# Kernel tuning notes

Measured on AMD Instinct MI355X. Metric: run time of the kernel, lower is better.

Reference implementation:

```python
import jax, jax.numpy as jnp
import numpy as np

B, T, C, V = 8, 2048, 1024, 32000


def setup_inputs() -> dict:
    key = jax.random.key(0)
    ks = jax.random.split(key, 12)
    s = 1.0 / np.sqrt(C)
    return {
        "input_tokens": jax.random.randint(ks[0], (B, T), 0, V),
        "xx_init": jnp.zeros((B, C), jnp.float32),
        "aa_init": jnp.zeros((B, C), jnp.float32),
        "bb_init": jnp.zeros((B, C), jnp.float32),
        "pp_init": jnp.zeros((B, C), jnp.float32),  # with aa=bb=0 this is equivalent to -inf init
        "emb": jax.random.normal(ks[1], (V, C), jnp.float32) * 0.02,
        "time_mix_k": jax.random.uniform(ks[2], (C,), jnp.float32),
        "time_mix_v": jax.random.uniform(ks[3], (C,), jnp.float32),
        "time_mix_r": jax.random.uniform(ks[4], (C,), jnp.float32),
        "time_decay": jax.random.normal(ks[5], (C,), jnp.float32) * 0.1,
        "time_first": jax.random.normal(ks[6], (C,), jnp.float32) * 0.1,
        "Wk": jax.random.normal(ks[7], (C, C), jnp.float32) * s,
        "Wv": jax.random.normal(ks[8], (C, C), jnp.float32) * s,
        "Wr": jax.random.normal(ks[9], (C, C), jnp.float32) * s,
        "Wo": jax.random.normal(ks[10], (C, C), jnp.float32) * s,
    }


def _wkv_scan(k, v, aa0, bb0, pp0, w, u):
    """Numerically-stable RWKV WKV recurrence.
    k, v: [T, B, C]; aa0/bb0/pp0: [B, C]; w (decay, negative), u (bonus): [C]."""
    def step(carry, kv):
        aa, bb, pp = carry
        kt, vt = kv
        ww = u + kt
        p = jnp.maximum(pp, ww)
        e1 = jnp.exp(pp - p)
        e2 = jnp.exp(ww - p)
        wkv = (e1 * aa + e2 * vt) / (e1 * bb + e2)
        ww2 = pp + w
        p2 = jnp.maximum(ww2, kt)
        e1b = jnp.exp(ww2 - p2)
        e2b = jnp.exp(kt - p2)
        return (e1b * aa + e2b * vt, e1b * bb + e2b, p2), wkv
    (aa, bb, pp), out = jax.lax.scan(step, (aa0, bb0, pp0), (k, v))
    return out, aa, bb, pp


def _forward(input_tokens, xx_init, aa_init, bb_init, pp_init, emb,
             time_mix_k, time_mix_v, time_mix_r, time_decay, time_first,
             Wk, Wv, Wr, Wo):
    x = emb[input_tokens]                                   # [B, T, C]
    xprev = jnp.concatenate([xx_init[:, None, :], x[:, :-1]], axis=1)  # token shift
    xk = x * time_mix_k + xprev * (1.0 - time_mix_k)
    xv = x * time_mix_v + xprev * (1.0 - time_mix_v)
    xr = x * time_mix_r + xprev * (1.0 - time_mix_r)
    k = jnp.einsum("btc,dc->btd", xk, Wk)
    v = jnp.einsum("btc,dc->btd", xv, Wv)
    r = jax.nn.sigmoid(jnp.einsum("btc,dc->btd", xr, Wr))
    w = -jnp.exp(time_decay)                                # per-channel decay
    u = time_first
    wkv, _, _, _ = _wkv_scan(jnp.swapaxes(k, 0, 1), jnp.swapaxes(v, 0, 1),
                             aa_init, bb_init, pp_init, w, u)
    wkv = jnp.swapaxes(wkv, 0, 1)                           # [B, T, C]
    rwkv = jnp.einsum("btc,dc->btd", r * wkv, Wo)
    e1 = rwkv[:, -1]          # final-step state
    e2 = rwkv.mean(axis=1)    # time-averaged state
    hx = (e1 + e2) * 0.5
    return jnp.stack([hx, hx])  # (hx, cx) stacked -> [2, B, C]


def reference(input_tokens, xx_init, aa_init, bb_init, pp_init, emb,
              time_mix_k, time_mix_v, time_mix_r, time_decay, time_first,
              Wk, Wv, Wr, Wo):
    return _forward(input_tokens, xx_init, aa_init, bb_init, pp_init, emb,
                    time_mix_k, time_mix_v, time_mix_r, time_decay, time_first,
                    Wk, Wv, Wr, Wo)
```

## Files before the change

kernel.cpp:

```cpp
#include <hip/hip_runtime.h>

#define Bdim 8
#define Tdim 2048
#define Cdim 1024
#define CHUNK 64
#define NCHUNK 32
#define BC (Bdim*Cdim)

typedef float floatx4 __attribute__((ext_vector_type(4)));
typedef _Float16 half8 __attribute__((ext_vector_type(8)));
typedef _Float16 half4v __attribute__((ext_vector_type(4)));
typedef _Float16 half2v __attribute__((ext_vector_type(2)));

__device__ __forceinline__ void load16(const void* g, void* l) {
    __builtin_amdgcn_global_load_lds(
        (const __attribute__((address_space(1))) void*)g,
        (__attribute__((address_space(3))) void*)l, 16, 0, 0);
}

__global__ __launch_bounds__(256) void mix_wconv(const int* __restrict__ tokens,
                                                 const float* __restrict__ xx_init,
                                                 const float* __restrict__ emb,
                                                 const float* __restrict__ tmk,
                                                 const float* __restrict__ tmv,
                                                 const float* __restrict__ tmr,
                                                 const float* __restrict__ Wk,
                                                 const float* __restrict__ Wv,
                                                 const float* __restrict__ Wr,
                                                 _Float16* __restrict__ xk,
                                                 _Float16* __restrict__ xv,
                                                 _Float16* __restrict__ xr,
                                                 _Float16* __restrict__ Wh) {
    int blk = blockIdx.x;
    if (blk < Bdim * Tdim) {
        int row = blk;
        int b = row >> 11;
        int t = row & (Tdim - 1);
        const float* cur = emb + (size_t)tokens[row] * Cdim;
        const float* prv = (t == 0) ? (xx_init + (size_t)b * Cdim)
                                    : (emb + (size_t)tokens[row - 1] * Cdim);
        int c = threadIdx.x * 4;
        float4 cu = *reinterpret_cast<const float4*>(cur + c);
        float4 pv = *reinterpret_cast<const float4*>(prv + c);
        float4 mk = *reinterpret_cast<const float4*>(tmk + c);
        float4 mv = *reinterpret_cast<const float4*>(tmv + c);
        float4 mr = *reinterpret_cast<const float4*>(tmr + c);
        float cf[4] = {cu.x, cu.y, cu.z, cu.w};
        float pf[4] = {pv.x, pv.y, pv.z, pv.w};
        float mkf[4] = {mk.x, mk.y, mk.z, mk.w};
        float mvf[4] = {mv.x, mv.y, mv.z, mv.w};
        float mrf[4] = {mr.x, mr.y, mr.z, mr.w};
        half4v hk, hv, hr;
        #pragma unroll
        for (int j = 0; j < 4; j++) {
            hk[j] = (_Float16)(mkf[j] * cf[j] + (1.0f - mkf[j]) * pf[j]);
            hv[j] = (_Float16)(mvf[j] * cf[j] + (1.0f - mvf[j]) * pf[j]);
            hr[j] = (_Float16)(mrf[j] * cf[j] + (1.0f - mrf[j]) * pf[j]);
        }
        size_t o = (size_t)row * Cdim + c;
        *reinterpret_cast<half4v*>(xk + o) = hk;
        *reinterpret_cast<half4v*>(xv + o) = hv;
        *reinterpret_cast<half4v*>(xr + o) = hr;
    } else {
        int idx2 = blk - Bdim * Tdim;
        int which = idx2 >> 10;
        const float* W = which == 0 ? Wk : (which == 1 ? Wv : Wr);
        _Float16* dst = Wh + (size_t)which * Cdim * Cdim;
        int i = ((idx2 & 1023) * 256 + threadIdx.x) * 4;
        float4 f = *reinterpret_cast<const float4*>(W + i);
        half4v h;
        h[0] = (_Float16)f.x; h[1] = (_Float16)f.y; h[2] = (_Float16)f.z; h[3] = (_Float16)f.w;
        *reinterpret_cast<half4v*>(dst + i) = h;
    }
}

__global__ __launch_bounds__(512, 2) void gemm_kvr(const _Float16* __restrict__ xk,
                                                   const _Float16* __restrict__ xv,
                                                   const _Float16* __restrict__ xr,
                                                   const _Float16* __restrict__ Wh,
                                                   _Float16* __restrict__ ko,
                                                   _Float16* __restrict__ vo,
                                                   _Float16* __restrict__ ro) {
    const int which = blockIdx.y;
    const _Float16* X = which == 0 ? xk : (which == 1 ? xv : xr);
    const _Float16* W = Wh + (size_t)which * Cdim * Cdim;
    _Float16* out     = which == 0 ? ko : (which == 1 ? vo : ro);

    const int lin = blockIdx.x;
    const int xcd = lin & 7;
    const int loc = lin >> 3;
    const int mt = xcd * 8 + (loc >> 2);
    const int nt = loc & 3;
    const int m0 = mt * 256;
    const int n0 = nt * 256;

    __shared__ _Float16 As[4 * 8192];
    __shared__ _Float16 Bs[4 * 8192];

    const int tid = threadIdx.x;
    const int lane = tid & 63;
    const int wave = tid >> 6;
    const int wm = (wave >> 2) * 128;
    const int wn = (wave & 3) * 64;
    const int lr = lane & 15;
    const int lk = lane >> 4;
    const int sw = (lr >> 1) & 3;

    const _Float16* Asrc = X + (size_t)m0 * Cdim;
    const _Float16* Bsrc = W + (size_t)n0 * Cdim;

    floatx4 acc[8][4] = {};

    auto stageA = [&](int kt) {
        const int p = kt & 3;
        const int k0 = kt * 32;
        #pragma unroll
        for (int i = 0; i < 2; i++) {
            int e = i * 512 + tid;
            int r = e >> 2;
            int cp = e & 3;
            int cl = cp ^ ((r >> 1) & 3);
            load16(Asrc + (size_t)r * Cdim + k0 + cl * 8, (char*)(As + p * 8192) + e * 16);
        }
    };
    auto stageB = [&](int kt) {
        const int p = kt & 3;
        const int k0 = kt * 32;
        #pragma unroll
        for (int i = 0; i < 2; i++) {
            int e = i * 512 + tid;
            int r = e >> 2;
            int cp = e & 3;
            int cl = cp ^ ((r >> 1) & 3);
            load16(Bsrc + (size_t)r * Cdim + k0 + cl * 8, (char*)(Bs + p * 8192) + e * 16);
        }
    };

    auto ktile = [&](int kt, bool st) {
        const int p = kt & 3;
        const _Float16* ap = As + p * 8192 + (wm + lr) * 32 + (lk ^ sw) * 8;
        const _Float16* bp = Bs + p * 8192 + (wn + lr) * 32 + (lk ^ sw) * 8;
        half8 af[8], bf[4];
        #pragma unroll
        for (int mi = 0; mi < 4; mi++)
            af[mi] = *reinterpret_cast<const half8*>(ap + mi * 512);
        #pragma unroll
        for (int ni = 0; ni < 4; ni++)
            bf[ni] = *reinterpret_cast<const half8*>(bp + ni * 512);
        if (st) stageA(kt + 3);
        __builtin_amdgcn_s_barrier();
        asm volatile("s_waitcnt lgkmcnt(0)" ::: "memory");
        __builtin_amdgcn_sched_barrier(0);
        __builtin_amdgcn_s_setprio(1);
        #pragma unroll
        for (int mi = 0; mi < 4; mi++)
            #pragma unroll
            for (int ni = 0; ni < 4; ni++)
                acc[mi][ni] = __builtin_amdgcn_mfma_f32_16x16x32_f16(af[mi], bf[ni], acc[mi][ni], 0, 0, 0);
        __builtin_amdgcn_s_setprio(0);
        __builtin_amdgcn_sched_barrier(0);
        __builtin_amdgcn_s_barrier();
        #pragma unroll
        for (int mi = 4; mi < 8; mi++)
            af[mi] = *reinterpret_cast<const half8*>(ap + mi * 512);
        if (st) stageB(kt + 3);
        __builtin_amdgcn_s_barrier();
        asm volatile("s_waitcnt lgkmcnt(0)" ::: "memory");
        __builtin_amdgcn_sched_barrier(0);
        __builtin_amdgcn_s_setprio(1);
        #pragma unroll
        for (int mi = 4; mi < 8; mi++)
            #pragma unroll
            for (int ni = 0; ni < 4; ni++)
                acc[mi][ni] = __builtin_amdgcn_mfma_f32_16x16x32_f16(af[mi], bf[ni], acc[mi][ni], 0, 0, 0);
        __builtin_amdgcn_s_setprio(0);
        __builtin_amdgcn_sched_barrier(0);
    };

    stageA(0); stageB(0); stageA(1); stageB(1); stageA(2); stageB(2);
    asm volatile("s_waitcnt vmcnt(8)" ::: "memory");
    __builtin_amdgcn_s_barrier();

    for (int kt = 0; kt < 29; ++kt) {
        ktile(kt, true);
        asm volatile("s_waitcnt vmcnt(8)" ::: "memory");
        __builtin_amdgcn_s_barrier();
    }
    ktile(29, false);
    asm volatile("s_waitcnt vmcnt(4)" ::: "memory");
    __builtin_amdgcn_s_barrier();
    ktile(30, false);
    asm volatile("s_waitcnt vmcnt(0)" ::: "memory");
    __builtin_amdgcn_s_barrier();
    ktile(31, false);

    #pragma unroll
    for (int mi = 0; mi < 8; mi++) {
        #pragma unroll
        for (int ni = 0; ni < 4; ni++) {
            #pragma unroll
            for (int reg = 0; reg < 4; reg++) {
                int mm = m0 + wm + mi * 16 + (lane >> 4) * 4 + reg;
                int nn = n0 + wn + ni * 16 + (lane & 15);
                float v = acc[mi][ni][reg];
                if (which == 2) v = 1.0f / (1.0f + __expf(-v));
                out[(size_t)mm * Cdim + nn] = (_Float16)v;
            }
        }
    }
}

__global__ __launch_bounds__(256) void scan_pass1(const _Float16* __restrict__ kb,
                                                  const _Float16* __restrict__ vb,
                                                  const float* __restrict__ tdecay,
                                                  float* __restrict__ tot_a,
                                                  float* __restrict__ tot_b,
                                                  float* __restrict__ tot_p) {
    const int idx = blockIdx.x * 256 + threadIdx.x;
    const int j  = idx >> 12;
    const int pc = idx & 4095;
    const int bc = pc * 2;
    const int b  = bc >> 10;
    const int c  = bc & (Cdim - 1);
    const float w0 = -__expf(tdecay[c]);
    const float w1 = -__expf(tdecay[c + 1]);
    const size_t base = ((size_t)(b * Tdim + j * CHUNK)) * Cdim + c;
    float aa0 = 0.0f, bb0 = 0.0f, pp0 = -1e30f;
    float aa1 = 0.0f, bb1 = 0.0f, pp1 = -1e30f;
    const _Float16* kp = kb + base;
    const _Float16* vp = vb + base;
    #pragma unroll 4
    for (int t = 0; t < CHUNK; t++) {
        half2v k2 = *reinterpret_cast<const half2v*>(kp + (size_t)t * Cdim);
        half2v v2 = *reinterpret_cast<const half2v*>(vp + (size_t)t * Cdim);
        {
            float kt = (float)k2[0], vt = (float)v2[0];
            float ww2 = pp0 + w0;
            float p2 = fmaxf(ww2, kt);
            float e1 = __expf(ww2 - p2);
            float e2 = __expf(kt - p2);
            aa0 = e1 * aa0 + e2 * vt; bb0 = e1 * bb0 + e2; pp0 = p2;
        }
        {
            float kt = (float)k2[1], vt = (float)v2[1];
            float ww2 = pp1 + w1;
            float p2 = fmaxf(ww2, kt);
            float e1 = __expf(ww2 - p2);
            float e2 = __expf(kt - p2);
            aa1 = e1 * aa1 + e2 * vt; bb1 = e1 * bb1 + e2; pp1 = p2;
        }
    }
    int o = j * BC + bc;
    *reinterpret_cast<float2*>(tot_a + o) = make_float2(aa0, aa1);
    *reinterpret_cast<float2*>(tot_b + o) = make_float2(bb0, bb1);
    *reinterpret_cast<float2*>(tot_p + o) = make_float2(pp0, pp1);
}

__global__ __launch_bounds__(256) void scan_pass2c(const _Float16* __restrict__ kb,
                                                   const _Float16* __restrict__ vb,
                                                   const _Float16* __restrict__ rb,
                                                   const float* __restrict__ tdecay,
                                                   const float* __restrict__ tfirst,
                                                   const float* __restrict__ aa_init,
                                                   const float* __restrict__ bb_init,
                                                   const float* __restrict__ pp_init,
                                                   const float* __restrict__ tot_a,
                                                   const float* __restrict__ tot_b,
                                                   const float* __restrict__ tot_p,
                                                   float* __restrict__ partial,
                                                   float* __restrict__ ylast) {
    const int idx = blockIdx.x * 256 + threadIdx.x;
    const int j  = idx >> 12;
    const int pc = idx & 4095;
    const int bc = pc * 2;
    const int b  = bc >> 10;
    const int c  = bc & (Cdim - 1);
    const float w0 = -__expf(tdecay[c]);
    const float w1 = -__expf(tdecay[c + 1]);
    const float wL0 = w0 * (float)CHUNK;
    const float wL1 = w1 * (float)CHUNK;
    const float u0 = tfirst[c], u1 = tfirst[c + 1];

    float2 A = *reinterpret_cast<const float2*>(aa_init + bc);
    float2 Bv = *reinterpret_cast<const float2*>(bb_init + bc);
    float2 P = *reinterpret_cast<const float2*>(pp_init + bc);
    float aa0 = A.x, bb0 = Bv.x, pp0 = P.x;
    float aa1 = A.y, bb1 = Bv.y, pp1 = P.y;
    for (int jj = 0; jj < j; jj++) {
        int o = jj * BC + bc;
        float2 ta = *reinterpret_cast<const float2*>(tot_a + o);
        float2 tb = *reinterpret_cast<const float2*>(tot_b + o);
        float2 tp = *reinterpret_cast<const float2*>(tot_p + o);
        {
            float px = pp0 + wL0;
            float q = fmaxf(px, tp.x);
            float e1 = __expf(px - q), e2 = __expf(tp.x - q);
            aa0 = e1 * aa0 + e2 * ta.x; bb0 = e1 * bb0 + e2 * tb.x; pp0 = q;
        }
        {
            float px = pp1 + wL1;
            float q = fmaxf(px, tp.y);
            float e1 = __expf(px - q), e2 = __expf(tp.y - q);
            aa1 = e1 * aa1 + e2 * ta.y; bb1 = e1 * bb1 + e2 * tb.y; pp1 = q;
        }
    }

    const size_t base = ((size_t)(b * Tdim + j * CHUNK)) * Cdim + c;
    const _Float16* kp = kb + base;
    const _Float16* vp = vb + base;
    const _Float16* rp = rb + base;
    float sum0 = 0.0f, sum1 = 0.0f, ylv0 = 0.0f, ylv1 = 0.0f;
    #pragma unroll 4
    for (int t = 0; t < CHUNK; t++) {
        half2v k2 = *reinterpret_cast<const half2v*>(kp + (size_t)t * Cdim);
        half2v v2 = *reinterpret_cast<const half2v*>(vp + (size_t)t * Cdim);
        half2v r2 = *reinterpret_cast<const half2v*>(rp + (size_t)t * Cdim);
        {
            float kt = (float)k2[0], vt = (float)v2[0], rt = (float)r2[0];
            float ww = u0 + kt;
            float p = fmaxf(pp0, ww);
            float e1 = __expf(pp0 - p), e2 = __expf(ww - p);
            float wkv = (e1 * aa0 + e2 * vt) / (e1 * bb0 + e2);
            float y = rt * wkv;
            sum0 += y; ylv0 = y;
            float ww2 = pp0 + w0;
            float p2 = fmaxf(ww2, kt);
            float e1b = __expf(ww2 - p2), e2b = __expf(kt - p2);
            aa0 = e1b * aa0 + e2b * vt; bb0 = e1b * bb0 + e2b; pp0 = p2;
        }
        {
            float kt = (float)k2[1], vt = (float)v2[1], rt = (float)r2[1];
            float ww = u1 + kt;
            float p = fmaxf(pp1, ww);
            float e1 = __expf(pp1 - p), e2 = __expf(ww - p);
            float wkv = (e1 * aa1 + e2 * vt) / (e1 * bb1 + e2);
            float y = rt * wkv;
            sum1 += y; ylv1 = y;
            float ww2 = pp1 + w1;
            float p2 = fmaxf(ww2, kt);
            float e1b = __expf(ww2 - p2), e2b = __expf(kt - p2);
            aa1 = e1b * aa1 + e2b * vt; bb1 = e1b * bb1 + e2b; pp1 = p2;
        }
    }
    int o = j * BC + bc;
    *reinterpret_cast<float2*>(partial + o) = make_float2(sum0, sum1);
    if (j == NCHUNK - 1)
        *reinterpret_cast<float2*>(ylast + bc) = make_float2(ylv0, ylv1);
}

__global__ __launch_bounds__(256) void reduce_z(const float* __restrict__ partial,
                                                const float* __restrict__ ylast,
                                                float* __restrict__ z) {
    int idx = blockIdx.x * 256 + threadIdx.x;
    int bc = idx * 2;
    float s0 = 0.0f, s1 = 0.0f;
    #pragma unroll 4
    for (int jj = 0; jj < NCHUNK; jj++) {
        float2 pr = *reinterpret_cast<const float2*>(partial + jj * BC + bc);
        s0 += pr.x; s1 += pr.y;
    }
    float2 yl = *reinterpret_cast<const float2*>(ylast + bc);
    float2 zv;
    zv.x = 0.5f * (yl.x + s0 * (1.0f / (float)Tdim));
    zv.y = 0.5f * (yl.y + s1 * (1.0f / (float)Tdim));
    *reinterpret_cast<float2*>(z + bc) = zv;
}

__global__ __launch_bounds__(256) void final_out(const float* __restrict__ z,
                                                 const float* __restrict__ Wo,
                                                 float* __restrict__ out) {
    int gw = (blockIdx.x * 256 + threadIdx.x) >> 6;
    int lane = threadIdx.x & 63;
    int b = gw >> 10;
    int d = gw & (Cdim - 1);
    const float* zr = z + (size_t)b * Cdim;
    const float* wr = Wo + (size_t)d * Cdim;
    float acc = 0.0f;
    #pragma unroll
    for (int i = lane; i < Cdim; i += 64) acc += zr[i] * wr[i];
    #pragma unroll
    for (int off = 32; off > 0; off >>= 1) acc += __shfl_down(acc, off);
    if (lane == 0) {
        out[(size_t)b * Cdim + d] = acc;
        out[(size_t)BC + (size_t)b * Cdim + d] = acc;
    }
}

extern "C" void kernel_launch(void* const* d_in, const int* in_sizes, int n_in,
                              void* d_out, int out_size, void* d_ws, size_t ws_size,
                              hipStream_t stream) {
    const int*   tokens  = (const int*)d_in[0];
    const float* xx_init = (const float*)d_in[1];
    const float* aa_init = (const float*)d_in[2];
    const float* bb_init = (const float*)d_in[3];
    const float* pp_init = (const float*)d_in[4];
    const float* emb     = (const float*)d_in[5];
    const float* tmk     = (const float*)d_in[6];
    const float* tmv     = (const float*)d_in[7];
    const float* tmr     = (const float*)d_in[8];
    const float* tdecay  = (const float*)d_in[9];
    const float* tfirst  = (const float*)d_in[10];
    const float* Wk      = (const float*)d_in[11];
    const float* Wv      = (const float*)d_in[12];
    const float* Wr      = (const float*)d_in[13];
    const float* Wo      = (const float*)d_in[14];
    float* out = (float*)d_out;

    char* ws = (char*)d_ws;
    size_t off = 0;
    auto alloc = [&](size_t bytes) -> void* {
        void* p = ws + off;
        off += (bytes + 255) & ~(size_t)255;
        return p;
    };
    _Float16* xkb = (_Float16*)alloc((size_t)Bdim * Tdim * Cdim * 2);
    _Float16* xvb = (_Float16*)alloc((size_t)Bdim * Tdim * Cdim * 2);
    _Float16* xrb = (_Float16*)alloc((size_t)Bdim * Tdim * Cdim * 2);
    _Float16* kb  = (_Float16*)alloc((size_t)Bdim * Tdim * Cdim * 2);
    _Float16* vb  = (_Float16*)alloc((size_t)Bdim * Tdim * Cdim * 2);
    _Float16* rb  = (_Float16*)alloc((size_t)Bdim * Tdim * Cdim * 2);
    _Float16* Wh = (_Float16*)alloc((size_t)3 * Cdim * Cdim * 2);
    float* tot_a = (float*)alloc((size_t)NCHUNK * BC * 4);
    float* tot_b = (float*)alloc((size_t)NCHUNK * BC * 4);
    float* tot_p = (float*)alloc((size_t)NCHUNK * BC * 4);
    float* partial = (float*)alloc((size_t)NCHUNK * BC * 4);
    float* ylast   = (float*)alloc((size_t)BC * 4);
    float* zbuf    = (float*)alloc((size_t)BC * 4);

    mix_wconv<<<Bdim * Tdim + 3072, 256, 0, stream>>>(tokens, xx_init, emb, tmk, tmv, tmr,
                                                      Wk, Wv, Wr, xkb, xvb, xrb, Wh);
    gemm_kvr<<<dim3(256, 3), 512, 0, stream>>>(xkb, xvb, xrb, Wh, kb, vb, rb);
    scan_pass1<<<(NCHUNK * BC / 2) / 256, 256, 0, stream>>>(kb, vb, tdecay, tot_a, tot_b, tot_p);
    scan_pass2c<<<(NCHUNK * BC / 2) / 256, 256, 0, stream>>>(kb, vb, rb, tdecay, tfirst,
                                                             aa_init, bb_init, pp_init,
                                                             tot_a, tot_b, tot_p, partial, ylast);
    reduce_z<<<(BC / 2) / 256, 256, 0, stream>>>(partial, ylast, zbuf);
    final_out<<<(BC / 4), 256, 0, stream>>>(zbuf, Wo, out);
}
```

Baseline: 413.0 us.

## Replace 4-stage split-phase GEMM pipeline with simple double buffering

The kvr GEMM drops from a 4-deep LDS ring with A/B loads interleaved between two MFMA half-phases to a 2-buffer scheme: prefetch the next tile, compute the current one fully, then wait and barrier. LDS per block is halved and the launch bound asks for 4 blocks per CU, aiming for more occupancy to hide latency instead of deep software prefetching. The risk is less prefetch distance, a full vmcnt(0) drain every iteration, and register pressure from 128 accumulators under a tighter occupancy target, which may cause spills.

Result: slower. 1.339 ms (+224.2%).

```diff
diff --git a/kernel.cpp b/kernel.cpp
--- a/kernel.cpp
+++ b/kernel.cpp
@@ -74,7 +74,7 @@
     }
 }
 
-__global__ __launch_bounds__(512, 2) void gemm_kvr(const _Float16* __restrict__ xk,
+__global__ __launch_bounds__(512, 4) void gemm_kvr(const _Float16* __restrict__ xk,
                                                    const _Float16* __restrict__ xv,
                                                    const _Float16* __restrict__ xr,
                                                    const _Float16* __restrict__ Wh,
@@ -94,8 +94,8 @@
     const int m0 = mt * 256;
     const int n0 = nt * 256;
 
-    __shared__ _Float16 As[4 * 8192];
-    __shared__ _Float16 Bs[4 * 8192];
+    __shared__ _Float16 As[2 * 8192];
+    __shared__ _Float16 Bs[2 * 8192];
 
     const int tid = threadIdx.x;
     const int lane = tid & 63;
@@ -111,8 +111,8 @@
 
     floatx4 acc[8][4] = {};
 
-    auto stageA = [&](int kt) {
-        const int p = kt & 3;
+    auto stage = [&](int kt) {
+        const int p = kt & 1;
         const int k0 = kt * 32;
         #pragma unroll
         for (int i = 0; i < 2; i++) {
@@ -122,10 +122,6 @@
             int cl = cp ^ ((r >> 1) & 3);
             load16(Asrc + (size_t)r * Cdim + k0 + cl * 8, (char*)(As + p * 8192) + e * 16);
         }
-    };
-    auto stageB = [&](int kt) {
-        const int p = kt & 3;
-        const int k0 = kt * 32;
         #pragma unroll
         for (int i = 0; i < 2; i++) {
             int e = i * 512 + tid;
@@ -136,40 +132,22 @@
         }
     };
 
-    auto ktile = [&](int kt, bool st) {
-        const int p = kt & 3;
+    auto compute = [&](int kt) {
+        const int p = kt & 1;
         const _Float16* ap = As + p * 8192 + (wm + lr) * 32 + (lk ^ sw) * 8;
         const _Float16* bp = Bs + p * 8192 + (wn + lr) * 32 + (lk ^ sw) * 8;
         half8 af[8], bf[4];
         #pragma unroll
-        for (int mi = 0; mi < 4; mi++)
+        for (int mi = 0; mi < 8; mi++)
             af[mi] = *reinterpret_cast<const half8*>(ap + mi * 512);
         #pragma unroll
         for (int ni = 0; ni < 4; ni++)
             bf[ni] = *reinterpret_cast<const half8*>(bp + ni * 512);
-        if (st) stageA(kt + 3);
-        __builtin_amdgcn_s_barrier();
         asm volatile("s_waitcnt lgkmcnt(0)" ::: "memory");
         __builtin_amdgcn_sched_barrier(0);
         __builtin_amdgcn_s_setprio(1);
         #pragma unroll
-        for (int mi = 0; mi < 4; mi++)
-            #pragma unroll
-            for (int ni = 0; ni < 4; ni++)
-                acc[mi][ni] = __builtin_amdgcn_mfma_f32_16x16x32_f16(af[mi], bf[ni], acc[mi][ni], 0, 0, 0);
-        __builtin_amdgcn_s_setprio(0);
-        __builtin_amdgcn_sched_barrier(0);
-        __builtin_amdgcn_s_barrier();
-        #pragma unroll
-        for (int mi = 4; mi < 8; mi++)
-            af[mi] = *reinterpret_cast<const half8*>(ap + mi * 512);
-        if (st) stageB(kt + 3);
-        __builtin_amdgcn_s_barrier();
-        asm volatile("s_waitcnt lgkmcnt(0)" ::: "memory");
-        __builtin_amdgcn_sched_barrier(0);
-        __builtin_amdgcn_s_setprio(1);
-        #pragma unroll
-        for (int mi = 4; mi < 8; mi++)
+        for (int mi = 0; mi < 8; mi++)
             #pragma unroll
             for (int ni = 0; ni < 4; ni++)
                 acc[mi][ni] = __builtin_amdgcn_mfma_f32_16x16x32_f16(af[mi], bf[ni], acc[mi][ni], 0, 0, 0);
@@ -177,22 +155,16 @@
         __builtin_amdgcn_sched_barrier(0);
     };
 
-    stageA(0); stageB(0); stageA(1); stageB(1); stageA(2); stageB(2);
-    asm volatile("s_waitcnt vmcnt(8)" ::: "memory");
-    __builtin_amdgcn_s_barrier();
-
-    for (int kt = 0; kt < 29; ++kt) {
-        ktile(kt, true);
-        asm volatile("s_waitcnt vmcnt(8)" ::: "memory");
-        __builtin_amdgcn_s_barrier();
-    }
-    ktile(29, false);
-    asm volatile("s_waitcnt vmcnt(4)" ::: "memory");
-    __builtin_amdgcn_s_barrier();
-    ktile(30, false);
+    stage(0);
     asm volatile("s_waitcnt vmcnt(0)" ::: "memory");
     __builtin_amdgcn_s_barrier();
-    ktile(31, false);
+
+    for (int kt = 0; kt < 32; ++kt) {
+        if (kt < 31) stage(kt + 1);
+        compute(kt);
+        asm volatile("s_waitcnt vmcnt(0)" ::: "memory");
+        __builtin_amdgcn_s_barrier();
+    }
 
     #pragma unroll
     for (int mi = 0; mi < 8; mi++) {
```
